# Optimization experiments

Measured on AMD Instinct MI355X. Metric: run time of the kernel, lower is better.

Reference implementation:

```python
import jax, jax.numpy as jnp
import numpy as np

N_ATOMS = 20
LS_PER_ATOM = [0, 0, 1, 1, 2]   # two s, two p, one d shell per atom
N_PRIM = 8
N_COORDS = 131072


def cart_angulars(l):
    return np.array([[lx, ly, l - lx - ly]
                     for lx in range(l, -1, -1)
                     for ly in range(l - lx, -1, -1)], dtype=np.float32)


def fact2(n):
    n = int(n)
    if n <= 0:
        return 1.0
    r = 1.0
    while n > 1:
        r *= n
        n -= 2
    return r


# ---- static shell bookkeeping (grouped by angular momentum l) ----
SHELL_ATOM = np.array([a for a in range(N_ATOMS) for _ in LS_PER_ATOM])
SHELL_L = np.array([l for _ in range(N_ATOMS) for l in LS_PER_ATOM])
N_SHELLS = len(SHELL_L)
UNIQUE_LS = sorted(set(LS_PER_ATOM))

GROUPS = {}
for l in UNIQUE_LS:
    idx = np.where(SHELL_L == l)[0]
    ls = cart_angulars(l)  # [ncart, 3]
    anorms = 1.0 / np.sqrt(np.array(
        [np.prod([fact2(2 * int(e) - 1) for e in row]) for row in ls],
        dtype=np.float64))
    GROUPS[l] = (idx, ls, anorms.astype(np.float32))

NAO_CART = sum(len(GROUPS[l][1]) * len(GROUPS[l][0]) for l in UNIQUE_LS)  # 280
NAO_SPH = sum((2 * l + 1) * len(GROUPS[l][0]) for l in UNIQUE_LS)          # 260


def setup_inputs() -> dict:
    key = jax.random.key(0)
    k1, k2, k3, k4, k5, k6 = jax.random.split(key, 6)
    coords = jax.random.normal(k1, (N_COORDS, 3), dtype=jnp.float32) * 2.0
    centers = jax.random.normal(k2, (N_ATOMS, 3), dtype=jnp.float32) * 3.0
    # Gaussian exponents must be positive
    zetas = jax.random.uniform(k3, (N_SHELLS, N_PRIM), dtype=jnp.float32,
                               minval=0.2, maxval=3.0)
    coeffs = jax.random.normal(k4, (N_SHELLS, N_PRIM), dtype=jnp.float32)
    normalization = jax.random.uniform(k5, (NAO_CART,), dtype=jnp.float32,
                                       minval=0.5, maxval=1.5)
    cart2sph = jax.random.normal(k6, (NAO_CART, NAO_SPH), dtype=jnp.float32) * 0.3
    return {"coords": coords, "centers": centers, "zetas": zetas,
            "coeffs": coeffs, "normalization": normalization,
            "cart2sph": cart2sph}


def reference(coords, centers, zetas, coeffs, normalization, cart2sph):
    """Batched GTOBasis.eval_ao: [N,3] -> [N, nao_sph]."""
    n = coords.shape[0]
    pieces = []
    for l in UNIQUE_LS:
        idx, ls, anorms = GROUPS[l]
        c = centers[SHELL_ATOM[idx]]                 # [S, 3]
        rs = coords[:, None, :] - c[None]            # [N, S, 3]
        rs2 = jnp.sum(rs * rs, axis=-1)              # [N, S]
        # cartesian angular part: prod over xyz of rs**l_component
        ang = jnp.prod(rs[:, :, None, :] ** jnp.asarray(ls)[None, None],
                       axis=-1)                      # [N, S, ncart]
        ex = jnp.exp(-zetas[idx][None] * rs2[:, :, None])  # [N, S, nprim]
        rad = jnp.sum(coeffs[idx][None] * ex, axis=-1)     # [N, S]
        phis = jnp.asarray(anorms) * ang * rad[:, :, None]  # [N, S, ncart]
        pieces.append(phis.reshape(n, -1))
    aos = jnp.concatenate(pieces, axis=-1) * normalization  # [N, nao_cart]
    return jnp.dot(aos, cart2sph)                           # [N, nao_sph]
```

## Files before the change

### kernel.cpp

```cpp
#include <hip/hip_runtime.h>

typedef unsigned int uint;
typedef unsigned short ushort;
typedef __attribute__((ext_vector_type(8))) short short8;
typedef __attribute__((ext_vector_type(4))) float f32x4;
typedef __attribute__((ext_vector_type(2))) uint uint2v;

#define NSH   100
#define NPRIM 8
#define NAOC  280
#define NAOS  260
#define NATOM 20
#define KP    288
#define NKB   9
#define MT    32
#define NCOLP 272
#define BCH   (32 * NCOLP)
#define RSQRT3 0.57735026918962576f
#define LOG2E  1.4426950408889634f
#define EPS   276

#define O_RAD   0
#define O_AH    12800
#define O_AL    16896
#define O_ZETA  12800
#define O_COEF  16000
#define O_CEN   20992
#define O_CX    21312
#define O_CY    21440
#define O_CZ    21568
#define O_NORMF 21696
#define O_META  22848
#define POOLSZ  24000

__device__ __forceinline__ ushort bf16_rne(float x) {
    uint u = __float_as_uint(x);
    return (ushort)((u + 0x7FFFu + ((u >> 16) & 1u)) >> 16);
}
__device__ __forceinline__ float bf16_to_f(ushort h) {
    return __uint_as_float(((uint)h) << 16);
}
__device__ __forceinline__ uint cvt_pk_bf16(float a, float b) {
    uint r;
    asm("v_cvt_pk_bf16_f32 %0, %1, %2" : "=v"(r) : "v"(a), "v"(b));
    return r;
}

__device__ __forceinline__ int calc_meta(int k, float& anorm) {
    int shell = 0, atom = 0, s1 = 0, s2 = 0;
    anorm = 1.0f;
    if (k < 40) {
        atom = k >> 1; shell = 5 * atom + (k & 1);
    } else if (k < 160) {
        int i = k - 40; int ip = i / 3; int c = i - 3 * ip;
        atom = ip >> 1; shell = 5 * atom + 2 + (ip & 1); s1 = 1 + c;
    } else if (k < NAOC) {
        int i = k - 160; atom = i / 6; shell = 5 * atom + 4; int c = i - 6 * atom;
        if      (c == 0) { s1 = 1; s2 = 1; }
        else if (c == 1) { s1 = 1; s2 = 2; }
        else if (c == 2) { s1 = 1; s2 = 3; }
        else if (c == 3) { s1 = 2; s2 = 2; }
        else if (c == 4) { s1 = 2; s2 = 3; }
        else             { s1 = 3; s2 = 3; }
        if (c == 0 || c == 3 || c == 5) anorm = RSQRT3;
    }
    return shell | (atom << 7) | (s1 << 12) | (s2 << 14);
}

__global__ void prep_b(const float* __restrict__ c2s, const float* __restrict__ norm,
                       ushort* __restrict__ wsHi, ushort* __restrict__ wsLo,
                       int* __restrict__ wsMeta, float* __restrict__ wsNorm) {
    if (blockIdx.x == 0) {
        for (int k = threadIdx.x; k < KP; k += 256) {
            float an;
            int m = calc_meta(k, an);
            wsMeta[k] = m;
            wsNorm[k] = (k < NAOC ? norm[k] : 0.0f) * an;
        }
    }
    int id = blockIdx.x * 256 + threadIdx.x;
    if (id >= KP * NCOLP) return;
    int k = id / NCOLP, col = id % NCOLP;
    float v = (k < NAOC && col < NAOS) ? c2s[k * NAOS + col] : 0.0f;
    ushort hi = bf16_rne(v);
    ushort lo = bf16_rne(v - bf16_to_f(hi));
    int off = (k >> 5) * BCH +
              (((col >> 4) * 4 + ((k & 31) >> 3)) * 16 + (col & 15)) * 8 + (k & 7);
    wsHi[off] = hi;
    wsLo[off] = lo;
}

template <bool USEWS>
__global__ __launch_bounds__(256, 4) void gto_mfma(
    const float* __restrict__ coords, const float* __restrict__ centers,
    const float* __restrict__ zetas, const float* __restrict__ coeffs,
    const float* __restrict__ norm, const float* __restrict__ c2s,
    const ushort* __restrict__ wsHi, const ushort* __restrict__ wsLo,
    const int* __restrict__ wsMeta, const float* __restrict__ wsNorm,
    float* __restrict__ out, int n)
{
    __shared__ __align__(16) char smem[POOLSZ];
    float*  sRad  = (float*)(smem + O_RAD);
    float*  sZeta = (float*)(smem + O_ZETA);
    float*  sCoef = (float*)(smem + O_COEF);
    float4* sCen4 = (float4*)(smem + O_CEN);
    float*  sCx   = (float*)(smem + O_CX);
    float*  sCy   = (float*)(smem + O_CY);
    float*  sCz   = (float*)(smem + O_CZ);
    float*  sNormF= (float*)(smem + O_NORMF);
    int*    sMeta = (int*)(smem + O_META);

    const int t = threadIdx.x, lane = t & 63, w = t >> 6;
    const int lr = lane & 15, lg4 = lane >> 4;
    const int P0 = blockIdx.x * MT;

    for (int i = t; i < NSH * NPRIM; i += 256) {
        sZeta[i] = zetas[i] * LOG2E;
        sCoef[i] = coeffs[i];
    }
    if (t < NATOM)
        sCen4[t] = make_float4(centers[3 * t], centers[3 * t + 1], centers[3 * t + 2], 0.0f);
    if (t < MT * 3) {
        int gi = P0 * 3 + t;
        float v = (gi < 3 * n) ? coords[gi] : 0.0f;
        int p = t / 3, c = t - 3 * (t / 3);
        if (c == 0) sCx[p] = v; else if (c == 1) sCy[p] = v; else sCz[p] = v;
    }
    if (USEWS) {
        for (int i = t; i < KP; i += 256) { sMeta[i] = wsMeta[i]; sNormF[i] = wsNorm[i]; }
    } else {
        for (int k = t; k < KP; k += 256) {
            float an;
            sMeta[k] = calc_meta(k, an);
            sNormF[k] = (k < NAOC ? norm[k] : 0.0f) * an;
        }
    }
    __syncthreads();

    #pragma unroll 1
    for (int it = 0; it < (NSH * MT + 255) / 256; ++it) {
        int id = it * 256 + t;
        if (id < NSH * MT) {
            int s = id >> 5, p = id & 31;
            int a = s / 5;
            float4 ca = sCen4[a];
            float dx = sCx[p] - ca.x;
            float dy = sCy[p] - ca.y;
            float dz = sCz[p] - ca.z;
            float r2 = dx * dx + dy * dy + dz * dz;
            float4 z0 = *(const float4*)&sZeta[s * NPRIM];
            float4 z1 = *(const float4*)&sZeta[s * NPRIM + 4];
            float4 c0 = *(const float4*)&sCoef[s * NPRIM];
            float4 c1 = *(const float4*)&sCoef[s * NPRIM + 4];
            float rad = c0.x * __builtin_amdgcn_exp2f(-z0.x * r2);
            rad += c0.y * __builtin_amdgcn_exp2f(-z0.y * r2);
            rad += c0.z * __builtin_amdgcn_exp2f(-z0.z * r2);
            rad += c0.w * __builtin_amdgcn_exp2f(-z0.w * r2);
            rad += c1.x * __builtin_amdgcn_exp2f(-z1.x * r2);
            rad += c1.y * __builtin_amdgcn_exp2f(-z1.y * r2);
            rad += c1.z * __builtin_amdgcn_exp2f(-z1.z * r2);
            rad += c1.w * __builtin_amdgcn_exp2f(-z1.w * r2);
            sRad[s * MT + p] = rad;
        }
    }

    const int pA = t & 31, kg = t >> 5;
    auto buildA = [&](int kb2) {
        const float cxp = sCx[pA], cyp = sCy[pA], czp = sCz[pA];
        const int k0 = kb2 * 32 + kg * 4;
        int4   m4  = *(const int4*)&sMeta[k0];
        float4 nf4 = *(const float4*)&sNormF[k0];
        float v[4];
        const int   mk[4] = {m4.x, m4.y, m4.z, m4.w};
        const float nf[4] = {nf4.x, nf4.y, nf4.z, nf4.w};
        #pragma unroll
        for (int j = 0; j < 4; ++j) {
            int meta = mk[j];
            int s = meta & 127, a = (meta >> 7) & 31;
            int s1 = (meta >> 12) & 3, s2 = (meta >> 14) & 3;
            float4 ca = sCen4[a];
            float dx = cxp - ca.x, dy = cyp - ca.y, dz = czp - ca.z;
            float m1 = (s1 == 0) ? 1.0f : ((s1 == 1) ? dx : ((s1 == 2) ? dy : dz));
            float m2 = (s2 == 0) ? 1.0f : ((s2 == 1) ? dx : ((s2 == 2) ? dy : dz));
            v[j] = sRad[s * MT + pA] * (m1 * m2) * nf[j];
        }
        uint h01 = cvt_pk_bf16(v[0], v[1]);
        uint h23 = cvt_pk_bf16(v[2], v[3]);
        float r0 = v[0] - __uint_as_float(h01 << 16);
        float r1 = v[1] - __uint_as_float(h01 & 0xffff0000u);
        float r2 = v[2] - __uint_as_float(h23 << 16);
        float r3 = v[3] - __uint_as_float(h23 & 0xffff0000u);
        uint l01 = cvt_pk_bf16(r0, r1);
        uint l23 = cvt_pk_bf16(r2, r3);
        const int boff = (kb2 & 1) * 2048 + ((kg >> 1) * 512 + pA * 16 + (kg & 1) * 8);
        *(uint2v*)(smem + O_AH + boff) = (uint2v){h01, h23};
        *(uint2v*)(smem + O_AL + boff) = (uint2v){l01, l23};
    };

    __syncthreads();
    buildA(0);

    f32x4 acc[5][2];
    #pragma unroll
    for (int i = 0; i < 5; ++i)
        #pragma unroll
        for (int mt = 0; mt < 2; ++mt)
            acc[i][mt] = (f32x4){0.0f, 0.0f, 0.0f, 0.0f};

    for (int kb = 0; kb < NKB; ++kb) {
        __syncthreads();

        short8 aH[2], aL[2];
        #pragma unroll
        for (int mt = 0; mt < 2; ++mt) {
            int off = (kb & 1) * 2048 + (lg4 * 32 + mt * 16 + lr) * 16;
            aH[mt] = *(const short8*)(smem + O_AH + off);
            aL[mt] = *(const short8*)(smem + O_AL + off);
        }

        if (kb + 1 < NKB) buildA(kb + 1);

        #pragma unroll
        for (int i = 0; i < 5; ++i) {
            if (i < 4 || w == 0) {
                int nt = (i == 4) ? 16 : (w * 4 + i);
                short8 bh, bl;
                if (USEWS) {
                    bh = *(const short8*)(wsHi + (size_t)kb * BCH + (nt * 64 + lane) * 8);
                    bl = *(const short8*)(wsLo + (size_t)kb * BCH + (nt * 64 + lane) * 8);
                } else {
                    #pragma unroll
                    for (int j = 0; j < 8; ++j) {
                        int k = kb * 32 + lg4 * 8 + j;
                        int col = nt * 16 + lr;
                        float v = (k < NAOC && col < NAOS) ? c2s[k * NAOS + col] : 0.0f;
                        ushort hi = bf16_rne(v);
                        bh[j] = (short)hi;
                        bl[j] = (short)bf16_rne(v - bf16_to_f(hi));
                    }
                }
                #pragma unroll
                for (int mt = 0; mt < 2; ++mt)
                    acc[i][mt] = __builtin_amdgcn_mfma_f32_16x16x32_bf16(aH[mt], bh, acc[i][mt], 0, 0, 0);
                #pragma unroll
                for (int mt = 0; mt < 2; ++mt)
                    acc[i][mt] = __builtin_amdgcn_mfma_f32_16x16x32_bf16(aH[mt], bl, acc[i][mt], 0, 0, 0);
                #pragma unroll
                for (int mt = 0; mt < 2; ++mt)
                    acc[i][mt] = __builtin_amdgcn_mfma_f32_16x16x32_bf16(aL[mt], bh, acc[i][mt], 0, 0, 0);
            }
        }
    }

    float* ep = (float*)smem;
    #pragma unroll
    for (int mt = 0; mt < 2; ++mt) {
        __syncthreads();
        #pragma unroll
        for (int i = 0; i < 5; ++i) {
            if (i < 4 || w == 0) {
                int nt = (i == 4) ? 16 : (w * 4 + i);
                int col = nt * 16 + lr;
                #pragma unroll
                for (int r = 0; r < 4; ++r)
                    ep[(lg4 * 4 + r) * EPS + col] = acc[i][mt][r];
            }
        }
        __syncthreads();
        #pragma unroll
        for (int j = 0; j < 4; ++j) {
            int row = w + j * 4;
            int P = P0 + mt * 16 + row;
            if (P < n)
                *(float4*)&out[(size_t)P * NAOS + lane * 4] = *(const float4*)&ep[row * EPS + lane * 4];
        }
        if (w == 1 && lane < 16) {
            int P = P0 + mt * 16 + lane;
            if (P < n)
                *(float4*)&out[(size_t)P * NAOS + 256] = *(const float4*)&ep[lane * EPS + 256];
        }
    }
}

extern "C" void kernel_launch(void* const* d_in, const int* in_sizes, int n_in,
                              void* d_out, int out_size, void* d_ws, size_t ws_size,
                              hipStream_t stream) {
    const float* coords  = (const float*)d_in[0];
    const float* centers = (const float*)d_in[1];
    const float* zetas   = (const float*)d_in[2];
    const float* coeffs  = (const float*)d_in[3];
    const float* norm    = (const float*)d_in[4];
    const float* c2s     = (const float*)d_in[5];
    float* out = (float*)d_out;
    int n = in_sizes[0] / 3;
    int grid = (n + MT - 1) / MT;

    ushort* wsHi = (ushort*)d_ws;
    ushort* wsLo = wsHi + (size_t)KP * NCOLP;
    int*    wsMeta = (int*)(wsLo + (size_t)KP * NCOLP);
    float*  wsNorm = (float*)(wsMeta + KP);
    const size_t WS_NEED = (size_t)2 * KP * NCOLP * sizeof(ushort) + KP * 8;

    if (ws_size >= WS_NEED) {
        prep_b<<<(KP * NCOLP + 255) / 256, 256, 0, stream>>>(c2s, norm, wsHi, wsLo, wsMeta, wsNorm);
        gto_mfma<true><<<grid, 256, 0, stream>>>(coords, centers, zetas, coeffs, norm, c2s,
                                                 wsHi, wsLo, wsMeta, wsNorm, out, n);
    } else {
        gto_mfma<false><<<grid, 256, 0, stream>>>(coords, centers, zetas, coeffs, norm, c2s,
                                                  nullptr, nullptr, nullptr, nullptr, out, n);
    }
}
```

Before: 104.3 us.

## Reorder K by atom, build full A tile per atom up front, fold norm into B

The cartesian AO axis is permuted so each atom's 14 functions are contiguous, and the matching rows of cart2sph (scaled by normalization and the d-shell angular norm) are permuted in the prep kernel. Each thread group now computes radial parts and angular products for whole atoms in registers and writes the complete bf16 hi/lo A tile to shared memory once. This removes the per-k meta decode, the sRad staging, and the per-iteration barriers in the K loop. In exchange, LDS use grows to about 44 KB per block, which may reduce occupancy, and the work per thread group is uneven (3 atoms vs 2).

```diff
diff --git a/kernel.cpp b/kernel.cpp
--- a/kernel.cpp
+++ b/kernel.cpp
@@ -4,7 +4,6 @@
 typedef unsigned short ushort;
 typedef __attribute__((ext_vector_type(8))) short short8;
 typedef __attribute__((ext_vector_type(4))) float f32x4;
-typedef __attribute__((ext_vector_type(2))) uint uint2v;
 
 #define NSH   100
 #define NPRIM 8
@@ -14,24 +13,22 @@
 #define KP    288
 #define NKB   9
 #define MT    32
+#define NTHR  256
 #define NCOLP 272
 #define BCH   (32 * NCOLP)
 #define RSQRT3 0.57735026918962576f
 #define LOG2E  1.4426950408889634f
 #define EPS   276
 
-#define O_RAD   0
-#define O_AH    12800
-#define O_AL    16896
-#define O_ZETA  12800
-#define O_COEF  16000
-#define O_CEN   20992
-#define O_CX    21312
-#define O_CY    21440
-#define O_CZ    21568
-#define O_NORMF 21696
-#define O_META  22848
-#define POOLSZ  24000
+#define O_AH    0
+#define O_AL    18432
+#define O_ZETA  36864
+#define O_COEF  40064
+#define O_CEN   43264
+#define O_CX    43584
+#define O_CY    43712
+#define O_CZ    43840
+#define POOLSZ  43968
 
 __device__ __forceinline__ ushort bf16_rne(float x) {
     uint u = __float_as_uint(x);
@@ -46,42 +43,27 @@
     return r;
 }
 
-__device__ __forceinline__ int calc_meta(int k, float& anorm) {
-    int shell = 0, atom = 0, s1 = 0, s2 = 0;
-    anorm = 1.0f;
-    if (k < 40) {
-        atom = k >> 1; shell = 5 * atom + (k & 1);
-    } else if (k < 160) {
-        int i = k - 40; int ip = i / 3; int c = i - 3 * ip;
-        atom = ip >> 1; shell = 5 * atom + 2 + (ip & 1); s1 = 1 + c;
-    } else if (k < NAOC) {
-        int i = k - 160; atom = i / 6; shell = 5 * atom + 4; int c = i - 6 * atom;
-        if      (c == 0) { s1 = 1; s2 = 1; }
-        else if (c == 1) { s1 = 1; s2 = 2; }
-        else if (c == 2) { s1 = 1; s2 = 3; }
-        else if (c == 3) { s1 = 2; s2 = 2; }
-        else if (c == 4) { s1 = 2; s2 = 3; }
-        else             { s1 = 3; s2 = 3; }
-        if (c == 0 || c == 3 || c == 5) anorm = RSQRT3;
-    }
-    return shell | (atom << 7) | (s1 << 12) | (s2 << 14);
+__device__ __forceinline__ float b_src(const float* __restrict__ c2s,
+                                       const float* __restrict__ norm,
+                                       int kp, int col) {
+    if (kp >= NAOC || col >= NAOS) return 0.0f;
+    int a = kp / 14, i = kp - 14 * a;
+    int ksrc; float an = 1.0f;
+    if (i < 2)      ksrc = 2 * a + i;
+    else if (i < 8) ksrc = 40 + 6 * a + (i - 2);
+    else {
+        ksrc = 160 + 6 * a + (i - 8);
+        if (i == 8 || i == 11 || i == 13) an = RSQRT3;
+    }
+    return c2s[ksrc * NAOS + col] * norm[ksrc] * an;
 }
 
 __global__ void prep_b(const float* __restrict__ c2s, const float* __restrict__ norm,
-                       ushort* __restrict__ wsHi, ushort* __restrict__ wsLo,
-                       int* __restrict__ wsMeta, float* __restrict__ wsNorm) {
-    if (blockIdx.x == 0) {
-        for (int k = threadIdx.x; k < KP; k += 256) {
-            float an;
-            int m = calc_meta(k, an);
-            wsMeta[k] = m;
-            wsNorm[k] = (k < NAOC ? norm[k] : 0.0f) * an;
-        }
-    }
+                       ushort* __restrict__ wsHi, ushort* __restrict__ wsLo) {
     int id = blockIdx.x * 256 + threadIdx.x;
     if (id >= KP * NCOLP) return;
     int k = id / NCOLP, col = id % NCOLP;
-    float v = (k < NAOC && col < NAOS) ? c2s[k * NAOS + col] : 0.0f;
+    float v = b_src(c2s, norm, k, col);
     ushort hi = bf16_rne(v);
     ushort lo = bf16_rne(v - bf16_to_f(hi));
     int off = (k >> 5) * BCH +
@@ -91,30 +73,26 @@
 }
 
 template <bool USEWS>
-__global__ __launch_bounds__(256, 4) void gto_mfma(
+__global__ __launch_bounds__(NTHR, 4) void gto_mfma(
     const float* __restrict__ coords, const float* __restrict__ centers,
     const float* __restrict__ zetas, const float* __restrict__ coeffs,
     const float* __restrict__ norm, const float* __restrict__ c2s,
     const ushort* __restrict__ wsHi, const ushort* __restrict__ wsLo,
-    const int* __restrict__ wsMeta, const float* __restrict__ wsNorm,
     float* __restrict__ out, int n)
 {
     __shared__ __align__(16) char smem[POOLSZ];
-    float*  sRad  = (float*)(smem + O_RAD);
     float*  sZeta = (float*)(smem + O_ZETA);
     float*  sCoef = (float*)(smem + O_COEF);
     float4* sCen4 = (float4*)(smem + O_CEN);
     float*  sCx   = (float*)(smem + O_CX);
     float*  sCy   = (float*)(smem + O_CY);
     float*  sCz   = (float*)(smem + O_CZ);
-    float*  sNormF= (float*)(smem + O_NORMF);
-    int*    sMeta = (int*)(smem + O_META);
 
     const int t = threadIdx.x, lane = t & 63, w = t >> 6;
     const int lr = lane & 15, lg4 = lane >> 4;
     const int P0 = blockIdx.x * MT;
 
-    for (int i = t; i < NSH * NPRIM; i += 256) {
+    for (int i = t; i < NSH * NPRIM; i += NTHR) {
         sZeta[i] = zetas[i] * LOG2E;
         sCoef[i] = coeffs[i];
     }
@@ -126,79 +104,62 @@
         int p = t / 3, c = t - 3 * (t / 3);
         if (c == 0) sCx[p] = v; else if (c == 1) sCy[p] = v; else sCz[p] = v;
     }
-    if (USEWS) {
-        for (int i = t; i < KP; i += 256) { sMeta[i] = wsMeta[i]; sNormF[i] = wsNorm[i]; }
-    } else {
-        for (int k = t; k < KP; k += 256) {
-            float an;
-            sMeta[k] = calc_meta(k, an);
-            sNormF[k] = (k < NAOC ? norm[k] : 0.0f) * an;
-        }
-    }
+    if (t < 64)        *(uint2*)(smem + O_AH + 35 * 512 + t * 8) = make_uint2(0u, 0u);
+    else if (t < 128)  *(uint2*)(smem + O_AL + 35 * 512 + (t - 64) * 8) = make_uint2(0u, 0u);
     __syncthreads();
 
-    #pragma unroll 1
-    for (int it = 0; it < (NSH * MT + 255) / 256; ++it) {
-        int id = it * 256 + t;
-        if (id < NSH * MT) {
-            int s = id >> 5, p = id & 31;
-            int a = s / 5;
-            float4 ca = sCen4[a];
-            float dx = sCx[p] - ca.x;
-            float dy = sCy[p] - ca.y;
-            float dz = sCz[p] - ca.z;
-            float r2 = dx * dx + dy * dy + dz * dz;
-            float4 z0 = *(const float4*)&sZeta[s * NPRIM];
-            float4 z1 = *(const float4*)&sZeta[s * NPRIM + 4];
-            float4 c0 = *(const float4*)&sCoef[s * NPRIM];
-            float4 c1 = *(const float4*)&sCoef[s * NPRIM + 4];
-            float rad = c0.x * __builtin_amdgcn_exp2f(-z0.x * r2);
-            rad += c0.y * __builtin_amdgcn_exp2f(-z0.y * r2);
-            rad += c0.z * __builtin_amdgcn_exp2f(-z0.z * r2);
-            rad += c0.w * __builtin_amdgcn_exp2f(-z0.w * r2);
-            rad += c1.x * __builtin_amdgcn_exp2f(-z1.x * r2);
-            rad += c1.y * __builtin_amdgcn_exp2f(-z1.y * r2);
-            rad += c1.z * __builtin_amdgcn_exp2f(-z1.z * r2);
-            rad += c1.w * __builtin_amdgcn_exp2f(-z1.w * r2);
-            sRad[s * MT + p] = rad;
-        }
-    }
-
-    const int pA = t & 31, kg = t >> 5;
-    auto buildA = [&](int kb2) {
-        const float cxp = sCx[pA], cyp = sCy[pA], czp = sCz[pA];
-        const int k0 = kb2 * 32 + kg * 4;
-        int4   m4  = *(const int4*)&sMeta[k0];
-        float4 nf4 = *(const float4*)&sNormF[k0];
-        float v[4];
-        const int   mk[4] = {m4.x, m4.y, m4.z, m4.w};
-        const float nf[4] = {nf4.x, nf4.y, nf4.z, nf4.w};
-        #pragma unroll
-        for (int j = 0; j < 4; ++j) {
-            int meta = mk[j];
-            int s = meta & 127, a = (meta >> 7) & 31;
-            int s1 = (meta >> 12) & 3, s2 = (meta >> 14) & 3;
-            float4 ca = sCen4[a];
-            float dx = cxp - ca.x, dy = cyp - ca.y, dz = czp - ca.z;
-            float m1 = (s1 == 0) ? 1.0f : ((s1 == 1) ? dx : ((s1 == 2) ? dy : dz));
-            float m2 = (s2 == 0) ? 1.0f : ((s2 == 1) ? dx : ((s2 == 2) ? dy : dz));
-            v[j] = sRad[s * MT + pA] * (m1 * m2) * nf[j];
-        }
-        uint h01 = cvt_pk_bf16(v[0], v[1]);
-        uint h23 = cvt_pk_bf16(v[2], v[3]);
-        float r0 = v[0] - __uint_as_float(h01 << 16);
-        float r1 = v[1] - __uint_as_float(h01 & 0xffff0000u);
-        float r2 = v[2] - __uint_as_float(h23 << 16);
-        float r3 = v[3] - __uint_as_float(h23 & 0xffff0000u);
-        uint l01 = cvt_pk_bf16(r0, r1);
-        uint l23 = cvt_pk_bf16(r2, r3);
-        const int boff = (kb2 & 1) * 2048 + ((kg >> 1) * 512 + pA * 16 + (kg & 1) * 8);
-        *(uint2v*)(smem + O_AH + boff) = (uint2v){h01, h23};
-        *(uint2v*)(smem + O_AL + boff) = (uint2v){l01, l23};
+    const int pA = t & 31, ag = t >> 5;
+    const float cxp = sCx[pA], cyp = sCy[pA], czp = sCz[pA];
+
+    auto doAtom = [&](int a) {
+        float4 ca = sCen4[a];
+        float dx = cxp - ca.x, dy = cyp - ca.y, dz = czp - ca.z;
+        float r2 = dx * dx + dy * dy + dz * dz;
+        float rad[5];
+        #pragma unroll
+        for (int sh = 0; sh < 5; ++sh) {
+            const float* z = &sZeta[(5 * a + sh) * NPRIM];
+            const float* cf = &sCoef[(5 * a + sh) * NPRIM];
+            float4 z0 = *(const float4*)z,  z1 = *(const float4*)(z + 4);
+            float4 c0 = *(const float4*)cf, c1 = *(const float4*)(cf + 4);
+            float r = c0.x * __builtin_amdgcn_exp2f(-z0.x * r2);
+            r += c0.y * __builtin_amdgcn_exp2f(-z0.y * r2);
+            r += c0.z * __builtin_amdgcn_exp2f(-z0.z * r2);
+            r += c0.w * __builtin_amdgcn_exp2f(-z0.w * r2);
+            r += c1.x * __builtin_amdgcn_exp2f(-z1.x * r2);
+            r += c1.y * __builtin_amdgcn_exp2f(-z1.y * r2);
+            r += c1.z * __builtin_amdgcn_exp2f(-z1.z * r2);
+            r += c1.w * __builtin_amdgcn_exp2f(-z1.w * r2);
+            rad[sh] = r;
+        }
+        float xx = dx * dx, xy = dx * dy, xz = dx * dz;
+        float yy = dy * dy, yz = dy * dz, zz = dz * dz;
+        float v[14] = { rad[0], rad[1],
+                        dx * rad[2], dy * rad[2], dz * rad[2],
+                        dx * rad[3], dy * rad[3], dz * rad[3],
+                        xx * rad[4], xy * rad[4], xz * rad[4],
+                        yy * rad[4], yz * rad[4], zz * rad[4] };
+        const int k0 = a * 14;
+        #pragma unroll
+        for (int pr = 0; pr < 7; ++pr) {
+            int k = k0 + 2 * pr;
+            uint h = cvt_pk_bf16(v[2 * pr], v[2 * pr + 1]);
+            float r0 = v[2 * pr]     - __uint_as_float(h << 16);
+            float r1 = v[2 * pr + 1] - __uint_as_float(h & 0xffff0000u);
+            uint l = cvt_pk_bf16(r0, r1);
+            const int off = (k >> 3) * 512 + pA * 16 + (k & 7) * 2;
+            *(uint*)(smem + O_AH + off) = h;
+            *(uint*)(smem + O_AL + off) = l;
+        }
     };
-
+    if (ag < 4) { doAtom(3 * ag); doAtom(3 * ag + 1); doAtom(3 * ag + 2); }
+    else        { int b = 12 + 2 * (ag - 4); doAtom(b); doAtom(b + 1); }
     __syncthreads();
-    buildA(0);
+
+    const ushort* pH  = wsHi + (4 * w * 64 + lane) * 8;
+    const ushort* pL  = wsLo + (4 * w * 64 + lane) * 8;
+    const ushort* pH2 = wsHi + (16 * 64 + lane) * 8;
+    const ushort* pL2 = wsLo + (16 * 64 + lane) * 8;
 
     f32x4 acc[5][2];
     #pragma unroll
@@ -207,33 +168,31 @@
         for (int mt = 0; mt < 2; ++mt)
             acc[i][mt] = (f32x4){0.0f, 0.0f, 0.0f, 0.0f};
 
+    #pragma unroll 1
     for (int kb = 0; kb < NKB; ++kb) {
-        __syncthreads();
-
         short8 aH[2], aL[2];
         #pragma unroll
         for (int mt = 0; mt < 2; ++mt) {
-            int off = (kb & 1) * 2048 + (lg4 * 32 + mt * 16 + lr) * 16;
+            const int off = (kb * 4 + lg4) * 512 + (mt * 16 + lr) * 16;
             aH[mt] = *(const short8*)(smem + O_AH + off);
             aL[mt] = *(const short8*)(smem + O_AL + off);
         }
-
-        if (kb + 1 < NKB) buildA(kb + 1);
-
         #pragma unroll
         for (int i = 0; i < 5; ++i) {
             if (i < 4 || w == 0) {
-                int nt = (i == 4) ? 16 : (w * 4 + i);
                 short8 bh, bl;
                 if (USEWS) {
-                    bh = *(const short8*)(wsHi + (size_t)kb * BCH + (nt * 64 + lane) * 8);
-                    bl = *(const short8*)(wsLo + (size_t)kb * BCH + (nt * 64 + lane) * 8);
+                    if (i < 4) { bh = *(const short8*)(pH + i * 512);
+                                 bl = *(const short8*)(pL + i * 512); }
+                    else       { bh = *(const short8*)pH2;
+                                 bl = *(const short8*)pL2; }
                 } else {
+                    int nt = (i == 4) ? 16 : (4 * w + i);
                     #pragma unroll
                     for (int j = 0; j < 8; ++j) {
                         int k = kb * 32 + lg4 * 8 + j;
                         int col = nt * 16 + lr;
-                        float v = (k < NAOC && col < NAOS) ? c2s[k * NAOS + col] : 0.0f;
+                        float v = b_src(c2s, norm, k, col);
                         ushort hi = bf16_rne(v);
                         bh[j] = (short)hi;
                         bl[j] = (short)bf16_rne(v - bf16_to_f(hi));
@@ -250,6 +209,7 @@
                     acc[i][mt] = __builtin_amdgcn_mfma_f32_16x16x32_bf16(aL[mt], bh, acc[i][mt], 0, 0, 0);
             }
         }
+        pH += BCH; pL += BCH; pH2 += BCH; pL2 += BCH;
     }
 
     float* ep = (float*)smem;
@@ -259,7 +219,7 @@
         #pragma unroll
         for (int i = 0; i < 5; ++i) {
             if (i < 4 || w == 0) {
-                int nt = (i == 4) ? 16 : (w * 4 + i);
+                int nt = (i == 4) ? 16 : (4 * w + i);
                 int col = nt * 16 + lr;
                 #pragma unroll
                 for (int r = 0; r < 4; ++r)
@@ -297,16 +257,14 @@
 
     ushort* wsHi = (ushort*)d_ws;
     ushort* wsLo = wsHi + (size_t)KP * NCOLP;
-    int*    wsMeta = (int*)(wsLo + (size_t)KP * NCOLP);
-    float*  wsNorm = (float*)(wsMeta + KP);
-    const size_t WS_NEED = (size_t)2 * KP * NCOLP * sizeof(ushort) + KP * 8;
+    const size_t WS_NEED = (size_t)2 * KP * NCOLP * sizeof(ushort);
 
     if (ws_size >= WS_NEED) {
-        prep_b<<<(KP * NCOLP + 255) / 256, 256, 0, stream>>>(c2s, norm, wsHi, wsLo, wsMeta, wsNorm);
-        gto_mfma<true><<<grid, 256, 0, stream>>>(coords, centers, zetas, coeffs, norm, c2s,
-                                                 wsHi, wsLo, wsMeta, wsNorm, out, n);
+        prep_b<<<(KP * NCOLP + 255) / 256, 256, 0, stream>>>(c2s, norm, wsHi, wsLo);
+        gto_mfma<true><<<grid, NTHR, 0, stream>>>(coords, centers, zetas, coeffs, norm, c2s,
+                                                  wsHi, wsLo, out, n);
     } else {
-        gto_mfma<false><<<grid, 256, 0, stream>>>(coords, centers, zetas, coeffs, norm, c2s,
-                                                  nullptr, nullptr, nullptr, nullptr, out, n);
-    }
-}
+        gto_mfma<false><<<grid, NTHR, 0, stream>>>(coords, centers, zetas, coeffs, norm, c2s,
+                                                   nullptr, nullptr, out, n);
+    }
+}
```

Result: faster. 91.88 us (-11.9%).
